# Performance work log

Hardware: AMD Instinct MI355X
Metric: run time of the kernel (lower is better)

## Reference

```python
import jax, jax.numpy as jnp
import numpy as np

B, S, D_IN, D_OUT = 8, 2048, 1024, 64

def setup_inputs() -> dict:
    key = jax.random.key(0)
    ks = jax.random.split(key, 6)
    return {
        "inputs_for_keys": jax.random.normal(ks[0], (B, S, D_IN), jnp.float32),
        "inputs_for_values": jax.random.normal(ks[1], (B, S, D_IN), jnp.float32),
        "inputs_for_queries": jax.random.normal(ks[2], (B, S, D_IN), jnp.float32),
        "K": jax.random.normal(ks[3], (D_IN, D_OUT), jnp.float32) * (1.0 / np.sqrt(D_IN)),
        "V": jax.random.normal(ks[4], (D_IN, D_OUT), jnp.float32) * (1.0 / np.sqrt(D_IN)),
        "Q": jax.random.normal(ks[5], (D_IN, D_OUT), jnp.float32) * (1.0 / np.sqrt(D_IN)),
    }

def reference(inputs_for_keys, inputs_for_values, inputs_for_queries, K, V, Q):
    # Project to per-head key/value/query spaces: [B, S, D_OUT]
    keys = jnp.einsum('bsd,de->bse', inputs_for_keys, K)
    values = jnp.einsum('bsd,de->bse', inputs_for_values, V)
    queries = jnp.einsum('bsd,de->bse', inputs_for_queries, Q)
    d_k = keys.shape[-1]
    # Scaled dot-product scores: [B, Sq, Sk]
    score = jnp.einsum('bqe,bke->bqk', queries, keys) / jnp.sqrt(jnp.float32(d_k))
    # Causal mask: -inf strictly above the diagonal (query i attends to keys <= i)
    sq, sk = score.shape[1], score.shape[2]
    causal = jnp.triu(jnp.full((sq, sk), -jnp.inf, dtype=score.dtype), k=1)
    score = score + causal[None, :, :]
    weights = jax.nn.softmax(score, axis=-1)
    # Attention output: [B, Sq, D_OUT]
    return jnp.einsum('bqk,bke->bqe', weights, values)
```

## Files before the change

kernel.cpp:

```cpp
#include <hip/hip_runtime.h>
#include <stdint.h>

#define BB   8
#define SS   2048
#define DIN  1024
#define DOUT 64

typedef __bf16 bf16_t;
typedef __bf16 bf16x8 __attribute__((ext_vector_type(8)));
typedef float  f32x4  __attribute__((ext_vector_type(4)));
typedef unsigned int u32x4 __attribute__((ext_vector_type(4)));

#define LOG2E 1.44269504088896f

__global__ void prep_weights(const float* __restrict__ Kw,
                             const float* __restrict__ Vw,
                             const float* __restrict__ Qw,
                             bf16_t* __restrict__ fw) {
    int proj = blockIdx.x >> 4;
    int seg  = blockIdx.x & 15;
    const float* W = (proj == 0) ? Kw : (proj == 1) ? Vw : Qw;
    float scale = (proj == 2) ? 0.125f : 1.0f;
    bf16_t* out = fw + proj * 65536;
    int base = seg * 4096;
#pragma unroll
    for (int i = 0; i < 16; ++i) {
        int idx  = base + i * 256 + threadIdx.x;
        int j    = idx & 7;
        int lane = (idx >> 3) & 63;
        int nt   = (idx >> 9) & 3;
        int kk   = idx >> 11;
        int k    = kk * 32 + (lane >> 4) * 8 + j;
        int col  = nt * 16 + (lane & 15);
        out[idx] = (bf16_t)(W[k * DOUT + col] * scale);
    }
}

__global__ __launch_bounds__(256) void proj_kernel(
    const float* __restrict__ Xk, const float* __restrict__ Xv,
    const float* __restrict__ Xq, const bf16_t* __restrict__ fw,
    bf16_t* __restrict__ outK, bf16_t* __restrict__ outV,
    bf16_t* __restrict__ outQ) {
    __shared__ __align__(16) bf16_t lds[16384];

    int proj = blockIdx.y;
    const float* X  = (proj == 0) ? Xk : (proj == 1) ? Xv : Xq;
    bf16_t* out     = (proj == 0) ? outK : (proj == 1) ? outV : outQ;
    const bf16_t* fwp = fw + proj * 65536;

    int tid  = threadIdx.x;
    int lane = tid & 63;
    int w    = tid >> 6;
    int row0 = blockIdx.x * 64 + w * 16;
    int arow = row0 + (lane & 15);
    const float* aptr = X + (size_t)arow * DIN + ((lane >> 4) * 8);

    f32x4 acc[4];
#pragma unroll
    for (int nt = 0; nt < 4; ++nt) acc[nt] = (f32x4)(0.0f);

    for (int c = 0; c < 4; ++c) {
        __syncthreads();
        const u32x4* src = (const u32x4*)(fwp + c * 16384);
        u32x4* dst = (u32x4*)lds;
#pragma unroll
        for (int i = 0; i < 8; ++i) dst[tid + 256 * i] = src[tid + 256 * i];
        __syncthreads();

#pragma unroll
        for (int kkl = 0; kkl < 8; ++kkl) {
            int kglob = c * 256 + kkl * 32;
            f32x4 a0 = *(const f32x4*)(aptr + kglob);
            f32x4 a1 = *(const f32x4*)(aptr + kglob + 4);
            bf16x8 af;
            af[0] = (bf16_t)a0[0]; af[1] = (bf16_t)a0[1];
            af[2] = (bf16_t)a0[2]; af[3] = (bf16_t)a0[3];
            af[4] = (bf16_t)a1[0]; af[5] = (bf16_t)a1[1];
            af[6] = (bf16_t)a1[2]; af[7] = (bf16_t)a1[3];
#pragma unroll
            for (int nt = 0; nt < 4; ++nt) {
                bf16x8 bfv = *(const bf16x8*)((const char*)lds +
                                ((size_t)((kkl * 4 + nt) * 64 + lane) * 16));
                acc[nt] = __builtin_amdgcn_mfma_f32_16x16x32_bf16(af, bfv, acc[nt], 0, 0, 0);
            }
        }
    }

#pragma unroll
    for (int nt = 0; nt < 4; ++nt) {
#pragma unroll
        for (int r = 0; r < 4; ++r) {
            int row = row0 + (lane >> 4) * 4 + r;
            int col = nt * 16 + (lane & 15);
            out[(size_t)row * DOUT + col] = (bf16_t)acc[nt][r];
        }
    }
}

__global__ __launch_bounds__(256) void attn_kernel(
    const bf16_t* __restrict__ Kp, const bf16_t* __restrict__ Vp,
    const bf16_t* __restrict__ Qp, float* __restrict__ out) {
    __shared__ __align__(16) bf16_t Klds[64 * 64];
    __shared__ __align__(16) bf16_t Vlds[64 * 64];
    __shared__ __align__(16) bf16_t Plds[4][16 * 64];

    int tid   = threadIdx.x;
    int lane  = tid & 63;
    int w     = tid >> 6;
    int qtile = blockIdx.x;
    int batch = blockIdx.y;

    const bf16_t* Kb = Kp + (size_t)batch * SS * DOUT;
    const bf16_t* Vb = Vp + (size_t)batch * SS * DOUT;
    const bf16_t* Qb = Qp + (size_t)batch * SS * DOUT;

    bf16x8 aq[2];
    {
        int r = qtile * 64 + w * 16 + (lane & 15);
        const bf16_t* qp = Qb + (size_t)r * DOUT + (lane >> 4) * 8;
        aq[0] = *(const bf16x8*)(qp);
        aq[1] = *(const bf16x8*)(qp + 32);
    }

    float m[4], lsum[4];
    f32x4 acc[4];
#pragma unroll
    for (int r = 0; r < 4; ++r) { m[r] = -1e30f; lsum[r] = 0.0f; }
#pragma unroll
    for (int nt = 0; nt < 4; ++nt) acc[nt] = (f32x4)(0.0f);

    int ntiles = qtile + 1;
    for (int j = 0; j < ntiles; ++j) {
        __syncthreads();
#pragma unroll
        for (int i = 0; i < 2; ++i) {
            int c   = tid + 256 * i;
            int key = c >> 3;
            int d0  = (c & 7) * 8;
            u32x4 v = *(const u32x4*)(Kb + ((size_t)(j * 64 + key)) * DOUT + d0);
            *(u32x4*)((char*)Klds + key * 128 + ((d0 * 2) ^ ((key & 7) << 4))) = v;
        }
#pragma unroll
        for (int i = 0; i < 2; ++i) {
            int c   = tid + 256 * i;
            int key = c >> 3;
            int d0  = (c & 7) * 8;
            bf16x8 v = *(const bf16x8*)(Vb + ((size_t)(j * 64 + key)) * DOUT + d0);
#pragma unroll
            for (int jj = 0; jj < 8; ++jj) {
                int d = d0 + jj;
                *(bf16_t*)((char*)Vlds + d * 128 + ((key * 2) ^ ((d & 7) << 4))) = v[jj];
            }
        }
        __syncthreads();

        f32x4 sfr[4];
#pragma unroll
        for (int nt = 0; nt < 4; ++nt) sfr[nt] = (f32x4)(0.0f);
#pragma unroll
        for (int kk = 0; kk < 2; ++kk) {
            int d0 = kk * 32 + (lane >> 4) * 8;
#pragma unroll
            for (int nt = 0; nt < 4; ++nt) {
                int key = nt * 16 + (lane & 15);
                bf16x8 bk = *(const bf16x8*)((char*)Klds + key * 128 +
                                             ((d0 * 2) ^ ((key & 7) << 4)));
                sfr[nt] = __builtin_amdgcn_mfma_f32_16x16x32_bf16(aq[kk], bk, sfr[nt], 0, 0, 0);
            }
        }

        if (j == qtile) {
#pragma unroll
            for (int nt = 0; nt < 4; ++nt) {
                int key = nt * 16 + (lane & 15);
#pragma unroll
                for (int r = 0; r < 4; ++r) {
                    int q = w * 16 + (lane >> 4) * 4 + r;
                    if (key > q) sfr[nt][r] = -1e30f;
                }
            }
        }

        float pf[4][4];
#pragma unroll
        for (int r = 0; r < 4; ++r) {
            float mx = fmaxf(fmaxf(sfr[0][r], sfr[1][r]), fmaxf(sfr[2][r], sfr[3][r]));
            mx = fmaxf(mx, __shfl_xor(mx, 1));
            mx = fmaxf(mx, __shfl_xor(mx, 2));
            mx = fmaxf(mx, __shfl_xor(mx, 4));
            mx = fmaxf(mx, __shfl_xor(mx, 8));
            float mn = fmaxf(m[r], mx);
            float scale = exp2f((m[r] - mn) * LOG2E);
            m[r] = mn;
            float rs = 0.0f;
#pragma unroll
            for (int nt = 0; nt < 4; ++nt) {
                float p = exp2f((sfr[nt][r] - mn) * LOG2E);
                pf[nt][r] = p;
                rs += p;
            }
            rs += __shfl_xor(rs, 1);
            rs += __shfl_xor(rs, 2);
            rs += __shfl_xor(rs, 4);
            rs += __shfl_xor(rs, 8);
            lsum[r] = lsum[r] * scale + rs;
#pragma unroll
            for (int nt = 0; nt < 4; ++nt) acc[nt][r] *= scale;
        }

#pragma unroll
        for (int nt = 0; nt < 4; ++nt) {
            int key = nt * 16 + (lane & 15);
#pragma unroll
            for (int r = 0; r < 4; ++r) {
                int q = (lane >> 4) * 4 + r;
                *(bf16_t*)((char*)&Plds[w][0] + q * 128 +
                           ((key * 2) ^ ((q & 7) << 4))) = (bf16_t)pf[nt][r];
            }
        }
        __syncthreads();

#pragma unroll
        for (int kk = 0; kk < 2; ++kk) {
            int k0 = kk * 32 + (lane >> 4) * 8;
            int q  = lane & 15;
            bf16x8 ap = *(const bf16x8*)((char*)&Plds[w][0] + q * 128 +
                                         ((k0 * 2) ^ ((q & 7) << 4)));
#pragma unroll
            for (int nt = 0; nt < 4; ++nt) {
                int d = nt * 16 + (lane & 15);
                bf16x8 bv = *(const bf16x8*)((char*)Vlds + d * 128 +
                                             ((k0 * 2) ^ ((d & 7) << 4)));
                acc[nt] = __builtin_amdgcn_mfma_f32_16x16x32_bf16(ap, bv, acc[nt], 0, 0, 0);
            }
        }
    }

    float* ob = out + ((size_t)batch * SS + qtile * 64 + w * 16) * DOUT;
#pragma unroll
    for (int nt = 0; nt < 4; ++nt) {
#pragma unroll
        for (int r = 0; r < 4; ++r) {
            int q = (lane >> 4) * 4 + r;
            int d = nt * 16 + (lane & 15);
            ob[(size_t)q * DOUT + d] = acc[nt][r] / lsum[r];
        }
    }
}

extern "C" void kernel_launch(void* const* d_in, const int* in_sizes, int n_in,
                              void* d_out, int out_size, void* d_ws, size_t ws_size,
                              hipStream_t stream) {
    const float* Xk = (const float*)d_in[0];
    const float* Xv = (const float*)d_in[1];
    const float* Xq = (const float*)d_in[2];
    const float* Kw = (const float*)d_in[3];
    const float* Vw = (const float*)d_in[4];
    const float* Qw = (const float*)d_in[5];

    bf16_t* Kp = (bf16_t*)d_ws;
    bf16_t* Vp = Kp + (size_t)BB * SS * DOUT;
    bf16_t* Qp = Vp + (size_t)BB * SS * DOUT;
    bf16_t* fw = Qp + (size_t)BB * SS * DOUT;

    prep_weights<<<dim3(48), dim3(256), 0, stream>>>(Kw, Vw, Qw, fw);
    proj_kernel<<<dim3(256, 3), dim3(256), 0, stream>>>(Xk, Xv, Xq, fw, Kp, Vp, Qp);
    attn_kernel<<<dim3(32, 8), dim3(256), 0, stream>>>(Kp, Vp, Qp, (float*)d_out);
}
```

Baseline: 109.5 us.

## Split-K projection across waves and split-KV attention with two key-tile groups

Measured after the change: 118.6 us. 1.08x slower.

```diff
diff --git a/kernel.cpp b/kernel.cpp
--- a/kernel.cpp
+++ b/kernel.cpp
@@ -36,90 +36,97 @@
     }
 }
 
-__global__ __launch_bounds__(256) void proj_kernel(
+__global__ __launch_bounds__(512) void proj_kernel(
     const float* __restrict__ Xk, const float* __restrict__ Xv,
     const float* __restrict__ Xq, const bf16_t* __restrict__ fw,
     bf16_t* __restrict__ outK, bf16_t* __restrict__ outV,
     bf16_t* __restrict__ outQ) {
-    __shared__ __align__(16) bf16_t lds[16384];
+    __shared__ float red[4][16][64];
+
+    int tid  = threadIdx.x;
+    int lane = tid & 63;
+    int w    = tid >> 6;
+    int wm   = w & 3;
+    int kh   = w >> 2;
 
     int proj = blockIdx.y;
     const float* X  = (proj == 0) ? Xk : (proj == 1) ? Xv : Xq;
     bf16_t* out     = (proj == 0) ? outK : (proj == 1) ? outV : outQ;
-    const bf16_t* fwp = fw + proj * 65536;
-
-    int tid  = threadIdx.x;
-    int lane = tid & 63;
-    int w    = tid >> 6;
-    int row0 = blockIdx.x * 64 + w * 16;
-    int arow = row0 + (lane & 15);
-    const float* aptr = X + (size_t)arow * DIN + ((lane >> 4) * 8);
+
+    int row0 = blockIdx.x * 64 + wm * 16;
+    const float* aptr = X + (size_t)(row0 + (lane & 15)) * DIN + kh * 512 + (lane >> 4) * 8;
+    const bf16_t* bptr = fw + proj * 65536 + kh * 32768 + lane * 8;
 
     f32x4 acc[4];
 #pragma unroll
     for (int nt = 0; nt < 4; ++nt) acc[nt] = (f32x4)(0.0f);
 
-    for (int c = 0; c < 4; ++c) {
-        __syncthreads();
-        const u32x4* src = (const u32x4*)(fwp + c * 16384);
-        u32x4* dst = (u32x4*)lds;
-#pragma unroll
-        for (int i = 0; i < 8; ++i) dst[tid + 256 * i] = src[tid + 256 * i];
-        __syncthreads();
-
-#pragma unroll
-        for (int kkl = 0; kkl < 8; ++kkl) {
-            int kglob = c * 256 + kkl * 32;
-            f32x4 a0 = *(const f32x4*)(aptr + kglob);
-            f32x4 a1 = *(const f32x4*)(aptr + kglob + 4);
-            bf16x8 af;
-            af[0] = (bf16_t)a0[0]; af[1] = (bf16_t)a0[1];
-            af[2] = (bf16_t)a0[2]; af[3] = (bf16_t)a0[3];
-            af[4] = (bf16_t)a1[0]; af[5] = (bf16_t)a1[1];
-            af[6] = (bf16_t)a1[2]; af[7] = (bf16_t)a1[3];
-#pragma unroll
-            for (int nt = 0; nt < 4; ++nt) {
-                bf16x8 bfv = *(const bf16x8*)((const char*)lds +
-                                ((size_t)((kkl * 4 + nt) * 64 + lane) * 16));
-                acc[nt] = __builtin_amdgcn_mfma_f32_16x16x32_bf16(af, bfv, acc[nt], 0, 0, 0);
-            }
-        }
-    }
-
-#pragma unroll
-    for (int nt = 0; nt < 4; ++nt) {
-#pragma unroll
-        for (int r = 0; r < 4; ++r) {
-            int row = row0 + (lane >> 4) * 4 + r;
-            int col = nt * 16 + (lane & 15);
-            out[(size_t)row * DOUT + col] = (bf16_t)acc[nt][r];
-        }
+#pragma unroll 2
+    for (int kk = 0; kk < 16; ++kk) {
+        f32x4 a0 = *(const f32x4*)(aptr + kk * 32);
+        f32x4 a1 = *(const f32x4*)(aptr + kk * 32 + 4);
+        bf16x8 b0 = *(const bf16x8*)(bptr + (kk * 4 + 0) * 512);
+        bf16x8 b1 = *(const bf16x8*)(bptr + (kk * 4 + 1) * 512);
+        bf16x8 b2 = *(const bf16x8*)(bptr + (kk * 4 + 2) * 512);
+        bf16x8 b3 = *(const bf16x8*)(bptr + (kk * 4 + 3) * 512);
+        bf16x8 af;
+        af[0] = (bf16_t)a0[0]; af[1] = (bf16_t)a0[1];
+        af[2] = (bf16_t)a0[2]; af[3] = (bf16_t)a0[3];
+        af[4] = (bf16_t)a1[0]; af[5] = (bf16_t)a1[1];
+        af[6] = (bf16_t)a1[2]; af[7] = (bf16_t)a1[3];
+        acc[0] = __builtin_amdgcn_mfma_f32_16x16x32_bf16(af, b0, acc[0], 0, 0, 0);
+        acc[1] = __builtin_amdgcn_mfma_f32_16x16x32_bf16(af, b1, acc[1], 0, 0, 0);
+        acc[2] = __builtin_amdgcn_mfma_f32_16x16x32_bf16(af, b2, acc[2], 0, 0, 0);
+        acc[3] = __builtin_amdgcn_mfma_f32_16x16x32_bf16(af, b3, acc[3], 0, 0, 0);
+    }
+
+    if (kh == 1) {
+#pragma unroll
+        for (int nt = 0; nt < 4; ++nt)
+#pragma unroll
+            for (int r = 0; r < 4; ++r)
+                red[wm][(lane >> 4) * 4 + r][nt * 16 + (lane & 15)] = acc[nt][r];
+    }
+    __syncthreads();
+    if (kh == 0) {
+#pragma unroll
+        for (int nt = 0; nt < 4; ++nt)
+#pragma unroll
+            for (int r = 0; r < 4; ++r) {
+                int rr = (lane >> 4) * 4 + r;
+                int cc = nt * 16 + (lane & 15);
+                float v = acc[nt][r] + red[wm][rr][cc];
+                out[(size_t)(row0 + rr) * DOUT + cc] = (bf16_t)v;
+            }
     }
 }
 
 __global__ __launch_bounds__(256) void attn_kernel(
     const bf16_t* __restrict__ Kp, const bf16_t* __restrict__ Vp,
     const bf16_t* __restrict__ Qp, float* __restrict__ out) {
-    __shared__ __align__(16) bf16_t Klds[64 * 64];
-    __shared__ __align__(16) bf16_t Vlds[64 * 64];
+    __shared__ __align__(16) bf16_t Klds[2][64 * 64];
+    __shared__ __align__(16) bf16_t Vlds[2][64 * 64];
     __shared__ __align__(16) bf16_t Plds[4][16 * 64];
 
     int tid   = threadIdx.x;
     int lane  = tid & 63;
     int w     = tid >> 6;
-    int qtile = blockIdx.x;
+    int g     = w >> 1;
+    int wq    = w & 1;
+    int gt    = tid & 127;
+    int qt    = blockIdx.x;
     int batch = blockIdx.y;
 
     const bf16_t* Kb = Kp + (size_t)batch * SS * DOUT;
     const bf16_t* Vb = Vp + (size_t)batch * SS * DOUT;
     const bf16_t* Qb = Qp + (size_t)batch * SS * DOUT;
 
-    bf16x8 aq[2];
+    bf16x8 aq0, aq1;
     {
-        int r = qtile * 64 + w * 16 + (lane & 15);
+        int r = qt * 32 + wq * 16 + (lane & 15);
         const bf16_t* qp = Qb + (size_t)r * DOUT + (lane >> 4) * 8;
-        aq[0] = *(const bf16x8*)(qp);
-        aq[1] = *(const bf16x8*)(qp + 32);
+        aq0 = *(const bf16x8*)(qp);
+        aq1 = *(const bf16x8*)(qp + 32);
     }
 
     float m[4], lsum[4];
@@ -129,30 +136,37 @@
 #pragma unroll
     for (int nt = 0; nt < 4; ++nt) acc[nt] = (f32x4)(0.0f);
 
-    int ntiles = qtile + 1;
-    for (int j = 0; j < ntiles; ++j) {
+    int dt     = qt >> 1;
+    int ntl    = dt + 1;
+    int imax   = (ntl + 1) >> 1;
+
+    char* Kl = (char*)&Klds[g][0];
+    char* Vl = (char*)&Vlds[g][0];
+
+    for (int i = 0; i < imax; ++i) {
+        int t = 2 * i + g;
+        bool act = t < ntl;
         __syncthreads();
-#pragma unroll
-        for (int i = 0; i < 2; ++i) {
-            int c   = tid + 256 * i;
-            int key = c >> 3;
-            int d0  = (c & 7) * 8;
-            u32x4 v = *(const u32x4*)(Kb + ((size_t)(j * 64 + key)) * DOUT + d0);
-            *(u32x4*)((char*)Klds + key * 128 + ((d0 * 2) ^ ((key & 7) << 4))) = v;
-        }
-#pragma unroll
-        for (int i = 0; i < 2; ++i) {
-            int c   = tid + 256 * i;
-            int key = c >> 3;
-            int d0  = (c & 7) * 8;
-            bf16x8 v = *(const bf16x8*)(Vb + ((size_t)(j * 64 + key)) * DOUT + d0);
-#pragma unroll
-            for (int jj = 0; jj < 8; ++jj) {
-                int d = d0 + jj;
-                *(bf16_t*)((char*)Vlds + d * 128 + ((key * 2) ^ ((d & 7) << 4))) = v[jj];
+        if (act) {
+            const bf16_t* Kt = Kb + (size_t)t * 64 * DOUT;
+            const bf16_t* Vt = Vb + (size_t)t * 64 * DOUT;
+#pragma unroll
+            for (int ii = 0; ii < 4; ++ii) {
+                int c   = gt + 128 * ii;
+                int key = c >> 3;
+                int d0  = (c & 7) * 8;
+                u32x4 kv = *(const u32x4*)(Kt + (size_t)key * DOUT + d0);
+                *(u32x4*)(Kl + key * 128 + ((d0 * 2) ^ ((key & 7) << 4))) = kv;
+                bf16x8 vv = *(const bf16x8*)(Vt + (size_t)key * DOUT + d0);
+#pragma unroll
+                for (int jj = 0; jj < 8; ++jj) {
+                    int d = d0 + jj;
+                    *(bf16_t*)(Vl + d * 128 + ((key * 2) ^ ((d & 7) << 4))) = vv[jj];
+                }
             }
         }
         __syncthreads();
+        if (!act) continue;
 
         f32x4 sfr[4];
 #pragma unroll
@@ -163,20 +177,21 @@
 #pragma unroll
             for (int nt = 0; nt < 4; ++nt) {
                 int key = nt * 16 + (lane & 15);
-                bf16x8 bk = *(const bf16x8*)((char*)Klds + key * 128 +
+                bf16x8 bk = *(const bf16x8*)(Kl + key * 128 +
                                              ((d0 * 2) ^ ((key & 7) << 4)));
-                sfr[nt] = __builtin_amdgcn_mfma_f32_16x16x32_bf16(aq[kk], bk, sfr[nt], 0, 0, 0);
-            }
-        }
-
-        if (j == qtile) {
-#pragma unroll
-            for (int nt = 0; nt < 4; ++nt) {
-                int key = nt * 16 + (lane & 15);
+                sfr[nt] = __builtin_amdgcn_mfma_f32_16x16x32_bf16(
+                              kk == 0 ? aq0 : aq1, bk, sfr[nt], 0, 0, 0);
+            }
+        }
+
+        if (t == dt) {
+#pragma unroll
+            for (int nt = 0; nt < 4; ++nt) {
+                int keyg = t * 64 + nt * 16 + (lane & 15);
 #pragma unroll
                 for (int r = 0; r < 4; ++r) {
-                    int q = w * 16 + (lane >> 4) * 4 + r;
-                    if (key > q) sfr[nt][r] = -1e30f;
+                    int qg = qt * 32 + wq * 16 + (lane >> 4) * 4 + r;
+                    if (keyg > qg) sfr[nt][r] = -1e30f;
                 }
             }
         }
@@ -218,7 +233,6 @@
                            ((key * 2) ^ ((q & 7) << 4))) = (bf16_t)pf[nt][r];
             }
         }
-        __syncthreads();
 
 #pragma unroll
         for (int kk = 0; kk < 2; ++kk) {
@@ -229,21 +243,48 @@
 #pragma unroll
             for (int nt = 0; nt < 4; ++nt) {
                 int d = nt * 16 + (lane & 15);
-                bf16x8 bv = *(const bf16x8*)((char*)Vlds + d * 128 +
+                bf16x8 bv = *(const bf16x8*)(Vl + d * 128 +
                                              ((k0 * 2) ^ ((d & 7) << 4)));
                 acc[nt] = __builtin_amdgcn_mfma_f32_16x16x32_bf16(ap, bv, acc[nt], 0, 0, 0);
             }
         }
     }
 
-    float* ob = out + ((size_t)batch * SS + qtile * 64 + w * 16) * DOUT;
-#pragma unroll
-    for (int nt = 0; nt < 4; ++nt) {
+    __syncthreads();
+    float* Olds = (float*)&Klds[0][0];
+    float* Ml   = (float*)&Vlds[0][0];
+    float* Ll   = Ml + 32;
+    if (g == 1) {
+#pragma unroll
+        for (int nt = 0; nt < 4; ++nt)
+#pragma unroll
+            for (int r = 0; r < 4; ++r)
+                Olds[(wq * 16 + (lane >> 4) * 4 + r) * 64 + nt * 16 + (lane & 15)] = acc[nt][r];
+        if ((lane & 15) == 0) {
+#pragma unroll
+            for (int r = 0; r < 4; ++r) {
+                int rr = wq * 16 + (lane >> 4) * 4 + r;
+                Ml[rr] = m[r];
+                Ll[rr] = lsum[r];
+            }
+        }
+    }
+    __syncthreads();
+    if (g == 0) {
+        float* ob = out + ((size_t)batch * SS + qt * 32) * DOUT;
 #pragma unroll
         for (int r = 0; r < 4; ++r) {
-            int q = (lane >> 4) * 4 + r;
-            int d = nt * 16 + (lane & 15);
-            ob[(size_t)q * DOUT + d] = acc[nt][r] / lsum[r];
+            int rr = wq * 16 + (lane >> 4) * 4 + r;
+            float m1 = Ml[rr], l1 = Ll[rr];
+            float mm = fmaxf(m[r], m1);
+            float e0 = exp2f((m[r] - mm) * LOG2E);
+            float e1 = exp2f((m1 - mm) * LOG2E);
+            float li = 1.0f / (lsum[r] * e0 + l1 * e1);
+#pragma unroll
+            for (int nt = 0; nt < 4; ++nt) {
+                int cc = nt * 16 + (lane & 15);
+                ob[(size_t)rr * DOUT + cc] = (acc[nt][r] * e0 + Olds[rr * 64 + cc] * e1) * li;
+            }
         }
     }
 }
@@ -264,6 +305,6 @@
     bf16_t* fw = Qp + (size_t)BB * SS * DOUT;
 
     prep_weights<<<dim3(48), dim3(256), 0, stream>>>(Kw, Vw, Qw, fw);
-    proj_kernel<<<dim3(256, 3), dim3(256), 0, stream>>>(Xk, Xv, Xq, fw, Kp, Vp, Qp);
-    attn_kernel<<<dim3(32, 8), dim3(256), 0, stream>>>(Kp, Vp, Qp, (float*)d_out);
+    proj_kernel<<<dim3(256, 3), dim3(512), 0, stream>>>(Xk, Xv, Xq, fw, Kp, Vp, Qp);
+    attn_kernel<<<dim3(64, 8), dim3(256), 0, stream>>>(Kp, Vp, Qp, (float*)d_out);
 }
```

## Double-buffer K/V tiles in attention, shrink query tiles, prefetch projection inputs

Applied to the files above, without the earlier changes.

Result: slower. 123.8 us (+13.0%).

```diff
diff --git a/kernel.cpp b/kernel.cpp
--- a/kernel.cpp
+++ b/kernel.cpp
@@ -10,6 +10,7 @@
 typedef __bf16 bf16x8 __attribute__((ext_vector_type(8)));
 typedef float  f32x4  __attribute__((ext_vector_type(4)));
 typedef unsigned int u32x4 __attribute__((ext_vector_type(4)));
+typedef unsigned short us8 __attribute__((ext_vector_type(8)));
 
 #define LOG2E 1.44269504088896f
 
@@ -36,90 +37,111 @@
     }
 }
 
-__global__ __launch_bounds__(256) void proj_kernel(
+__global__ __launch_bounds__(256, 2) void proj_kernel(
     const float* __restrict__ Xk, const float* __restrict__ Xv,
     const float* __restrict__ Xq, const bf16_t* __restrict__ fw,
     bf16_t* __restrict__ outK, bf16_t* __restrict__ outV,
     bf16_t* __restrict__ outQ) {
-    __shared__ __align__(16) bf16_t lds[16384];
+    __shared__ __align__(16) bf16_t Blds[32768];
+
+    int tid  = threadIdx.x;
+    int lane = tid & 63;
+    int w    = tid >> 6;
 
     int proj = blockIdx.y;
     const float* X  = (proj == 0) ? Xk : (proj == 1) ? Xv : Xq;
     bf16_t* out     = (proj == 0) ? outK : (proj == 1) ? outV : outQ;
     const bf16_t* fwp = fw + proj * 65536;
 
-    int tid  = threadIdx.x;
-    int lane = tid & 63;
-    int w    = tid >> 6;
     int row0 = blockIdx.x * 64 + w * 16;
-    int arow = row0 + (lane & 15);
-    const float* aptr = X + (size_t)arow * DIN + ((lane >> 4) * 8);
+    const float* aptr = X + (size_t)(row0 + (lane & 15)) * DIN + (lane >> 4) * 8;
 
     f32x4 acc[4];
 #pragma unroll
     for (int nt = 0; nt < 4; ++nt) acc[nt] = (f32x4)(0.0f);
 
-    for (int c = 0; c < 4; ++c) {
+    for (int kh = 0; kh < 2; ++kh) {
         __syncthreads();
-        const u32x4* src = (const u32x4*)(fwp + c * 16384);
-        u32x4* dst = (u32x4*)lds;
-#pragma unroll
-        for (int i = 0; i < 8; ++i) dst[tid + 256 * i] = src[tid + 256 * i];
+        {
+            const u32x4* src = (const u32x4*)(fwp + kh * 32768);
+            u32x4* dst = (u32x4*)Blds;
+#pragma unroll
+            for (int i = 0; i < 16; ++i) dst[tid + 256 * i] = src[tid + 256 * i];
+        }
         __syncthreads();
 
-#pragma unroll
-        for (int kkl = 0; kkl < 8; ++kkl) {
-            int kglob = c * 256 + kkl * 32;
-            f32x4 a0 = *(const f32x4*)(aptr + kglob);
-            f32x4 a1 = *(const f32x4*)(aptr + kglob + 4);
-            bf16x8 af;
-            af[0] = (bf16_t)a0[0]; af[1] = (bf16_t)a0[1];
-            af[2] = (bf16_t)a0[2]; af[3] = (bf16_t)a0[3];
-            af[4] = (bf16_t)a1[0]; af[5] = (bf16_t)a1[1];
-            af[6] = (bf16_t)a1[2]; af[7] = (bf16_t)a1[3];
-#pragma unroll
-            for (int nt = 0; nt < 4; ++nt) {
-                bf16x8 bfv = *(const bf16x8*)((const char*)lds +
-                                ((size_t)((kkl * 4 + nt) * 64 + lane) * 16));
-                acc[nt] = __builtin_amdgcn_mfma_f32_16x16x32_bf16(af, bfv, acc[nt], 0, 0, 0);
-            }
-        }
-    }
-
-#pragma unroll
-    for (int nt = 0; nt < 4; ++nt) {
+        const float* ah = aptr + kh * 512;
+        f32x4 a00 = *(const f32x4*)(ah);
+        f32x4 a01 = *(const f32x4*)(ah + 4);
+        f32x4 a10 = *(const f32x4*)(ah + 32);
+        f32x4 a11 = *(const f32x4*)(ah + 36);
+
+#pragma unroll
+        for (int kk = 0; kk < 16; kk += 2) {
+            f32x4 n00, n01, n10, n11;
+            if (kk < 14) {
+                n00 = *(const f32x4*)(ah + (kk + 2) * 32);
+                n01 = *(const f32x4*)(ah + (kk + 2) * 32 + 4);
+                n10 = *(const f32x4*)(ah + (kk + 3) * 32);
+                n11 = *(const f32x4*)(ah + (kk + 3) * 32 + 4);
+            }
+            bf16x8 af0;
+            af0[0] = (bf16_t)a00[0]; af0[1] = (bf16_t)a00[1];
+            af0[2] = (bf16_t)a00[2]; af0[3] = (bf16_t)a00[3];
+            af0[4] = (bf16_t)a01[0]; af0[5] = (bf16_t)a01[1];
+            af0[6] = (bf16_t)a01[2]; af0[7] = (bf16_t)a01[3];
+#pragma unroll
+            for (int nt = 0; nt < 4; ++nt) {
+                bf16x8 b = *(const bf16x8*)(Blds + ((kk * 4 + nt) * 512 + lane * 8));
+                acc[nt] = __builtin_amdgcn_mfma_f32_16x16x32_bf16(af0, b, acc[nt], 0, 0, 0);
+            }
+            bf16x8 af1;
+            af1[0] = (bf16_t)a10[0]; af1[1] = (bf16_t)a10[1];
+            af1[2] = (bf16_t)a10[2]; af1[3] = (bf16_t)a10[3];
+            af1[4] = (bf16_t)a11[0]; af1[5] = (bf16_t)a11[1];
+            af1[6] = (bf16_t)a11[2]; af1[7] = (bf16_t)a11[3];
+#pragma unroll
+            for (int nt = 0; nt < 4; ++nt) {
+                bf16x8 b = *(const bf16x8*)(Blds + (((kk + 1) * 4 + nt) * 512 + lane * 8));
+                acc[nt] = __builtin_amdgcn_mfma_f32_16x16x32_bf16(af1, b, acc[nt], 0, 0, 0);
+            }
+            a00 = n00; a01 = n01; a10 = n10; a11 = n11;
+        }
+    }
+
+#pragma unroll
+    for (int nt = 0; nt < 4; ++nt)
 #pragma unroll
         for (int r = 0; r < 4; ++r) {
-            int row = row0 + (lane >> 4) * 4 + r;
-            int col = nt * 16 + (lane & 15);
-            out[(size_t)row * DOUT + col] = (bf16_t)acc[nt][r];
-        }
-    }
+            int rr = (lane >> 4) * 4 + r;
+            int cc = nt * 16 + (lane & 15);
+            out[(size_t)(row0 + rr) * DOUT + cc] = (bf16_t)acc[nt][r];
+        }
 }
 
-__global__ __launch_bounds__(256) void attn_kernel(
+__global__ __launch_bounds__(128, 3) void attn_kernel(
     const bf16_t* __restrict__ Kp, const bf16_t* __restrict__ Vp,
     const bf16_t* __restrict__ Qp, float* __restrict__ out) {
-    __shared__ __align__(16) bf16_t Klds[64 * 64];
-    __shared__ __align__(16) bf16_t Vlds[64 * 64];
-    __shared__ __align__(16) bf16_t Plds[4][16 * 64];
+    __shared__ __align__(16) bf16_t Kl[2][64 * 64];
+    __shared__ __align__(16) bf16_t Vl[2][64 * 64];
+    __shared__ __align__(16) bf16_t Pl[2][16 * 64];
 
     int tid   = threadIdx.x;
     int lane  = tid & 63;
     int w     = tid >> 6;
-    int qtile = blockIdx.x;
+    int qt    = blockIdx.x;
     int batch = blockIdx.y;
 
     const bf16_t* Kb = Kp + (size_t)batch * SS * DOUT;
     const bf16_t* Vb = Vp + (size_t)batch * SS * DOUT;
     const bf16_t* Qb = Qp + (size_t)batch * SS * DOUT;
 
-    bf16x8 aq[2];
+    bf16x8 aq0, aq1;
     {
-        int r = qtile * 64 + w * 16 + (lane & 15);
+        int r = qt * 32 + w * 16 + (lane & 15);
         const bf16_t* qp = Qb + (size_t)r * DOUT + (lane >> 4) * 8;
-        aq[0] = *(const bf16x8*)(qp);
-        aq[1] = *(const bf16x8*)(qp + 32);
+        aq0 = *(const bf16x8*)(qp);
+        aq1 = *(const bf16x8*)(qp + 32);
     }
 
     float m[4], lsum[4];
@@ -129,30 +151,60 @@
 #pragma unroll
     for (int nt = 0; nt < 4; ++nt) acc[nt] = (f32x4)(0.0f);
 
-    int ntiles = qtile + 1;
-    for (int j = 0; j < ntiles; ++j) {
-        __syncthreads();
+    int dt  = qt >> 1;
+    int ntl = dt + 1;
+
+    {
+        const bf16_t* Kt = Kb;
+        const bf16_t* Vt = Vb;
+#pragma unroll
+        for (int i = 0; i < 4; ++i) {
+            int ch  = tid + 128 * i;
+            int key = ch >> 3;
+            int d0  = (ch & 7) * 8;
+            u32x4 kv = *(const u32x4*)(Kt + (size_t)key * DOUT + d0);
+            *(u32x4*)((char*)&Kl[0][0] + key * 128 + ((d0 * 2) ^ ((key & 7) << 4))) = kv;
+        }
 #pragma unroll
         for (int i = 0; i < 2; ++i) {
-            int c   = tid + 256 * i;
-            int key = c >> 3;
-            int d0  = (c & 7) * 8;
-            u32x4 v = *(const u32x4*)(Kb + ((size_t)(j * 64 + key)) * DOUT + d0);
-            *(u32x4*)((char*)Klds + key * 128 + ((d0 * 2) ^ ((key & 7) << 4))) = v;
-        }
-#pragma unroll
-        for (int i = 0; i < 2; ++i) {
-            int c   = tid + 256 * i;
-            int key = c >> 3;
-            int d0  = (c & 7) * 8;
-            bf16x8 v = *(const bf16x8*)(Vb + ((size_t)(j * 64 + key)) * DOUT + d0);
+            int vch  = tid + 128 * i;
+            int key0 = (vch >> 3) * 2;
+            int d0   = (vch & 7) * 8;
+            us8 va = *(const us8*)(Vt + (size_t)key0 * DOUT + d0);
+            us8 vb = *(const us8*)(Vt + (size_t)(key0 + 1) * DOUT + d0);
 #pragma unroll
             for (int jj = 0; jj < 8; ++jj) {
                 int d = d0 + jj;
-                *(bf16_t*)((char*)Vlds + d * 128 + ((key * 2) ^ ((d & 7) << 4))) = v[jj];
-            }
-        }
-        __syncthreads();
+                unsigned int pack = (unsigned int)va[jj] | ((unsigned int)vb[jj] << 16);
+                *(unsigned int*)((char*)&Vl[0][0] + d * 128 + ((key0 * 2) ^ ((d & 7) << 4))) = pack;
+            }
+        }
+    }
+    __syncthreads();
+
+    for (int t = 0; t < ntl; ++t) {
+        int cur = t & 1;
+        bool pf = (t + 1) < ntl;
+
+        u32x4 pk0, pk1, pk2, pk3;
+        us8 pva0, pvb0, pva1, pvb1;
+        int vkey0_0 = ((tid) >> 3) * 2,       vd0_0 = (tid & 7) * 8;
+        int vkey0_1 = ((tid + 128) >> 3) * 2, vd0_1 = (tid & 7) * 8;
+        if (pf) {
+            const bf16_t* Kt = Kb + (size_t)(t + 1) * 64 * DOUT;
+            const bf16_t* Vt = Vb + (size_t)(t + 1) * 64 * DOUT;
+            pk0 = *(const u32x4*)(Kt + (size_t)((tid) >> 3) * DOUT + (tid & 7) * 8);
+            pk1 = *(const u32x4*)(Kt + (size_t)((tid + 128) >> 3) * DOUT + (tid & 7) * 8);
+            pk2 = *(const u32x4*)(Kt + (size_t)((tid + 256) >> 3) * DOUT + (tid & 7) * 8);
+            pk3 = *(const u32x4*)(Kt + (size_t)((tid + 384) >> 3) * DOUT + (tid & 7) * 8);
+            pva0 = *(const us8*)(Vt + (size_t)vkey0_0 * DOUT + vd0_0);
+            pvb0 = *(const us8*)(Vt + (size_t)(vkey0_0 + 1) * DOUT + vd0_0);
+            pva1 = *(const us8*)(Vt + (size_t)vkey0_1 * DOUT + vd0_1);
+            pvb1 = *(const us8*)(Vt + (size_t)(vkey0_1 + 1) * DOUT + vd0_1);
+        }
+
+        char* Kc = (char*)&Kl[cur][0];
+        char* Vc = (char*)&Vl[cur][0];
 
         f32x4 sfr[4];
 #pragma unroll
@@ -163,25 +215,26 @@
 #pragma unroll
             for (int nt = 0; nt < 4; ++nt) {
                 int key = nt * 16 + (lane & 15);
-                bf16x8 bk = *(const bf16x8*)((char*)Klds + key * 128 +
+                bf16x8 bk = *(const bf16x8*)(Kc + key * 128 +
                                              ((d0 * 2) ^ ((key & 7) << 4)));
-                sfr[nt] = __builtin_amdgcn_mfma_f32_16x16x32_bf16(aq[kk], bk, sfr[nt], 0, 0, 0);
-            }
-        }
-
-        if (j == qtile) {
-#pragma unroll
-            for (int nt = 0; nt < 4; ++nt) {
-                int key = nt * 16 + (lane & 15);
+                sfr[nt] = __builtin_amdgcn_mfma_f32_16x16x32_bf16(
+                              kk == 0 ? aq0 : aq1, bk, sfr[nt], 0, 0, 0);
+            }
+        }
+
+        if (t == dt) {
+#pragma unroll
+            for (int nt = 0; nt < 4; ++nt) {
+                int keyg = t * 64 + nt * 16 + (lane & 15);
 #pragma unroll
                 for (int r = 0; r < 4; ++r) {
-                    int q = w * 16 + (lane >> 4) * 4 + r;
-                    if (key > q) sfr[nt][r] = -1e30f;
+                    int qg = qt * 32 + w * 16 + (lane >> 4) * 4 + r;
+                    if (keyg > qg) sfr[nt][r] = -1e30f;
                 }
             }
         }
 
-        float pf[4][4];
+        float pfv[4][4];
 #pragma unroll
         for (int r = 0; r < 4; ++r) {
             float mx = fmaxf(fmaxf(sfr[0][r], sfr[1][r]), fmaxf(sfr[2][r], sfr[3][r]));
@@ -196,7 +249,7 @@
 #pragma unroll
             for (int nt = 0; nt < 4; ++nt) {
                 float p = exp2f((sfr[nt][r] - mn) * LOG2E);
-                pf[nt][r] = p;
+                pfv[nt][r] = p;
                 rs += p;
             }
             rs += __shfl_xor(rs, 1);
@@ -214,38 +267,70 @@
 #pragma unroll
             for (int r = 0; r < 4; ++r) {
                 int q = (lane >> 4) * 4 + r;
-                *(bf16_t*)((char*)&Plds[w][0] + q * 128 +
-                           ((key * 2) ^ ((q & 7) << 4))) = (bf16_t)pf[nt][r];
-            }
-        }
-        __syncthreads();
+                *(bf16_t*)((char*)&Pl[w][0] + q * 128 +
+                           ((key * 2) ^ ((q & 7) << 4))) = (bf16_t)pfv[nt][r];
+            }
+        }
 
 #pragma unroll
         for (int kk = 0; kk < 2; ++kk) {
             int k0 = kk * 32 + (lane >> 4) * 8;
             int q  = lane & 15;
-            bf16x8 ap = *(const bf16x8*)((char*)&Plds[w][0] + q * 128 +
+            bf16x8 ap = *(const bf16x8*)((char*)&Pl[w][0] + q * 128 +
                                          ((k0 * 2) ^ ((q & 7) << 4)));
 #pragma unroll
             for (int nt = 0; nt < 4; ++nt) {
                 int d = nt * 16 + (lane & 15);
-                bf16x8 bv = *(const bf16x8*)((char*)Vlds + d * 128 +
+                bf16x8 bv = *(const bf16x8*)(Vc + d * 128 +
                                              ((k0 * 2) ^ ((d & 7) << 4)));
                 acc[nt] = __builtin_amdgcn_mfma_f32_16x16x32_bf16(ap, bv, acc[nt], 0, 0, 0);
             }
         }
-    }
-
-    float* ob = out + ((size_t)batch * SS + qtile * 64 + w * 16) * DOUT;
-#pragma unroll
-    for (int nt = 0; nt < 4; ++nt) {
+
+        if (pf) {
+            char* Kn = (char*)&Kl[cur ^ 1][0];
+            char* Vn = (char*)&Vl[cur ^ 1][0];
+            {
+                int key = (tid) >> 3, d0 = (tid & 7) * 8;
+                *(u32x4*)(Kn + key * 128 + ((d0 * 2) ^ ((key & 7) << 4))) = pk0;
+            }
+            {
+                int key = (tid + 128) >> 3, d0 = (tid & 7) * 8;
+                *(u32x4*)(Kn + key * 128 + ((d0 * 2) ^ ((key & 7) << 4))) = pk1;
+            }
+            {
+                int key = (tid + 256) >> 3, d0 = (tid & 7) * 8;
+                *(u32x4*)(Kn + key * 128 + ((d0 * 2) ^ ((key & 7) << 4))) = pk2;
+            }
+            {
+                int key = (tid + 384) >> 3, d0 = (tid & 7) * 8;
+                *(u32x4*)(Kn + key * 128 + ((d0 * 2) ^ ((key & 7) << 4))) = pk3;
+            }
+#pragma unroll
+            for (int jj = 0; jj < 8; ++jj) {
+                int d = vd0_0 + jj;
+                unsigned int pack = (unsigned int)pva0[jj] | ((unsigned int)pvb0[jj] << 16);
+                *(unsigned int*)(Vn + d * 128 + ((vkey0_0 * 2) ^ ((d & 7) << 4))) = pack;
+            }
+#pragma unroll
+            for (int jj = 0; jj < 8; ++jj) {
+                int d = vd0_1 + jj;
+                unsigned int pack = (unsigned int)pva1[jj] | ((unsigned int)pvb1[jj] << 16);
+                *(unsigned int*)(Vn + d * 128 + ((vkey0_1 * 2) ^ ((d & 7) << 4))) = pack;
+            }
+        }
+        __syncthreads();
+    }
+
+    float* ob = out + ((size_t)batch * SS + qt * 32 + w * 16) * DOUT;
+#pragma unroll
+    for (int nt = 0; nt < 4; ++nt)
 #pragma unroll
         for (int r = 0; r < 4; ++r) {
-            int q = (lane >> 4) * 4 + r;
-            int d = nt * 16 + (lane & 15);
-            ob[(size_t)q * DOUT + d] = acc[nt][r] / lsum[r];
-        }
-    }
+            int rr = (lane >> 4) * 4 + r;
+            int cc = nt * 16 + (lane & 15);
+            ob[(size_t)rr * DOUT + cc] = acc[nt][r] / lsum[r];
+        }
 }
 
 extern "C" void kernel_launch(void* const* d_in, const int* in_sizes, int n_in,
@@ -265,5 +350,5 @@
 
     prep_weights<<<dim3(48), dim3(256), 0, stream>>>(Kw, Vw, Qw, fw);
     proj_kernel<<<dim3(256, 3), dim3(256), 0, stream>>>(Xk, Xv, Xq, fw, Kp, Vp, Qp);
-    attn_kernel<<<dim3(32, 8), dim3(256), 0, stream>>>(Kp, Vp, Qp, (float*)d_out);
+    attn_kernel<<<dim3(64, 8), dim3(128), 0, stream>>>(Kp, Vp, Qp, (float*)d_out);
 }
```

## Restructure projection GEMM with LDS-staged activations and split-K across waves

Applied to the files above, without the earlier changes.

Measured after the change: 117.5 us. 7.3% more time.

```diff
diff --git a/kernel.cpp b/kernel.cpp
--- a/kernel.cpp
+++ b/kernel.cpp
@@ -7,6 +7,7 @@
 #define DOUT 64
 
 typedef __bf16 bf16_t;
+typedef __bf16 bf16x4 __attribute__((ext_vector_type(4)));
 typedef __bf16 bf16x8 __attribute__((ext_vector_type(8)));
 typedef float  f32x4  __attribute__((ext_vector_type(4)));
 typedef unsigned int u32x4 __attribute__((ext_vector_type(4)));
@@ -36,64 +37,76 @@
     }
 }
 
-__global__ __launch_bounds__(256) void proj_kernel(
+__global__ __launch_bounds__(256, 2) void proj_kernel(
     const float* __restrict__ Xk, const float* __restrict__ Xv,
     const float* __restrict__ Xq, const bf16_t* __restrict__ fw,
     bf16_t* __restrict__ outK, bf16_t* __restrict__ outV,
     bf16_t* __restrict__ outQ) {
-    __shared__ __align__(16) bf16_t lds[16384];
+    __shared__ __align__(128) char Alds[65536];
+
+    int tid  = threadIdx.x;
+    int lane = tid & 63;
+    int w    = tid >> 6;
 
     int proj = blockIdx.y;
     const float* X  = (proj == 0) ? Xk : (proj == 1) ? Xv : Xq;
     bf16_t* out     = (proj == 0) ? outK : (proj == 1) ? outV : outQ;
     const bf16_t* fwp = fw + proj * 65536;
 
-    int tid  = threadIdx.x;
-    int lane = tid & 63;
-    int w    = tid >> 6;
-    int row0 = blockIdx.x * 64 + w * 16;
-    int arow = row0 + (lane & 15);
-    const float* aptr = X + (size_t)arow * DIN + ((lane >> 4) * 8);
-
-    f32x4 acc[4];
-#pragma unroll
-    for (int nt = 0; nt < 4; ++nt) acc[nt] = (f32x4)(0.0f);
-
-    for (int c = 0; c < 4; ++c) {
-        __syncthreads();
-        const u32x4* src = (const u32x4*)(fwp + c * 16384);
-        u32x4* dst = (u32x4*)lds;
-#pragma unroll
-        for (int i = 0; i < 8; ++i) dst[tid + 256 * i] = src[tid + 256 * i];
-        __syncthreads();
-
-#pragma unroll
-        for (int kkl = 0; kkl < 8; ++kkl) {
-            int kglob = c * 256 + kkl * 32;
-            f32x4 a0 = *(const f32x4*)(aptr + kglob);
-            f32x4 a1 = *(const f32x4*)(aptr + kglob + 4);
-            bf16x8 af;
-            af[0] = (bf16_t)a0[0]; af[1] = (bf16_t)a0[1];
-            af[2] = (bf16_t)a0[2]; af[3] = (bf16_t)a0[3];
-            af[4] = (bf16_t)a1[0]; af[5] = (bf16_t)a1[1];
-            af[6] = (bf16_t)a1[2]; af[7] = (bf16_t)a1[3];
-#pragma unroll
-            for (int nt = 0; nt < 4; ++nt) {
-                bf16x8 bfv = *(const bf16x8*)((const char*)lds +
-                                ((size_t)((kkl * 4 + nt) * 64 + lane) * 16));
-                acc[nt] = __builtin_amdgcn_mfma_f32_16x16x32_bf16(af, bfv, acc[nt], 0, 0, 0);
-            }
-        }
-    }
-
-#pragma unroll
-    for (int nt = 0; nt < 4; ++nt) {
-#pragma unroll
-        for (int r = 0; r < 4; ++r) {
-            int row = row0 + (lane >> 4) * 4 + r;
-            int col = nt * 16 + (lane & 15);
-            out[(size_t)row * DOUT + col] = (bf16_t)acc[nt][r];
-        }
+    int row0 = blockIdx.x * 32;
+
+#pragma unroll
+    for (int j = 0; j < 32; ++j) {
+        f32x4 v = *(const f32x4*)(X + (size_t)(row0 + j) * DIN + tid * 4);
+        bf16x4 b;
+        b[0] = (bf16_t)v[0]; b[1] = (bf16_t)v[1];
+        b[2] = (bf16_t)v[2]; b[3] = (bf16_t)v[3];
+        *(bf16x4*)(Alds + j * 2048 + ((tid * 8) ^ ((j & 7) << 4))) = b;
+    }
+    __syncthreads();
+
+    f32x4 acc[2][4];
+#pragma unroll
+    for (int t = 0; t < 2; ++t)
+#pragma unroll
+        for (int nt = 0; nt < 4; ++nt) acc[t][nt] = (f32x4)(0.0f);
+
+    int arow = lane & 15;
+#pragma unroll
+    for (int kk = 0; kk < 8; ++kk) {
+        int k0 = w * 256 + kk * 32;
+        int kb = (k0 + (lane >> 4) * 8) * 2;
+        int sw = kb ^ ((arow & 7) << 4);
+        bf16x8 a0 = *(const bf16x8*)(Alds + arow * 2048 + sw);
+        bf16x8 a1 = *(const bf16x8*)(Alds + (arow + 16) * 2048 + sw);
+        const bf16_t* bp = fwp + (size_t)((k0 >> 5) * 4) * 512 + lane * 8;
+#pragma unroll
+        for (int nt = 0; nt < 4; ++nt) {
+            bf16x8 b = *(const bf16x8*)(bp + nt * 512);
+            acc[0][nt] = __builtin_amdgcn_mfma_f32_16x16x32_bf16(a0, b, acc[0][nt], 0, 0, 0);
+            acc[1][nt] = __builtin_amdgcn_mfma_f32_16x16x32_bf16(a1, b, acc[1][nt], 0, 0, 0);
+        }
+    }
+
+    __syncthreads();
+    float* red = (float*)Alds;
+#pragma unroll
+    for (int t = 0; t < 2; ++t)
+#pragma unroll
+        for (int nt = 0; nt < 4; ++nt)
+#pragma unroll
+            for (int r = 0; r < 4; ++r) {
+                int row = t * 16 + (lane >> 4) * 4 + r;
+                int col = nt * 16 + (lane & 15);
+                red[w * 2048 + row * 64 + col] = acc[t][nt][r];
+            }
+    __syncthreads();
+#pragma unroll
+    for (int i = 0; i < 8; ++i) {
+        int row = w * 8 + i;
+        float s = red[row * 64 + lane] + red[2048 + row * 64 + lane] +
+                  red[4096 + row * 64 + lane] + red[6144 + row * 64 + lane];
+        out[(size_t)(row0 + row) * DOUT + lane] = (bf16_t)s;
     }
 }
 
@@ -264,6 +277,6 @@
     bf16_t* fw = Qp + (size_t)BB * SS * DOUT;
 
     prep_weights<<<dim3(48), dim3(256), 0, stream>>>(Kw, Vw, Qw, fw);
-    proj_kernel<<<dim3(256, 3), dim3(256), 0, stream>>>(Xk, Xv, Xq, fw, Kp, Vp, Qp);
+    proj_kernel<<<dim3(512, 3), dim3(256), 0, stream>>>(Xk, Xv, Xq, fw, Kp, Vp, Qp);
     attn_kernel<<<dim3(32, 8), dim3(256), 0, stream>>>(Kp, Vp, Qp, (float*)d_out);
 }
```
